# Kernel optimization log

Hardware: AMD Instinct MI355X
Metric: run time of the kernel (lower is better)

The kernel has to match this reference:

```python
import jax, jax.numpy as jnp
import numpy as np
from jax import lax

C = 128
B, H, W = 8, 128, 128
HW = H * W


def _layernorm(x, w, b):
    # x: [b,c,h,w]; WithBias LN over channel dim c (matches to_3d -> LN(last dim=c) -> to_4d)
    mu = jnp.mean(x, axis=1, keepdims=True)
    var = jnp.mean((x - mu) ** 2, axis=1, keepdims=True)
    xn = (x - mu) / jnp.sqrt(var + 1e-5)
    return xn * w[None, :, None, None] + b[None, :, None, None]


def _conv1x1(x, w, b):
    # x: [b,c,h,w], w: [out,in]
    return jnp.einsum('bchw,oc->bohw', x, w) + b[None, :, None, None]


def _dwconv3(x, w, b):
    # depthwise 3x3, w: [c,1,3,3]
    c = x.shape[1]
    y = lax.conv_general_dilated(x, w, window_strides=(1, 1),
                                 padding=((1, 1), (1, 1)),
                                 feature_group_count=c,
                                 dimension_numbers=('NCHW', 'OIHW', 'NCHW'))
    return y + b[None, :, None, None]


def _l2norm(x):
    # torch F.normalize(dim=-1): x / max(||x||, 1e-12)
    n = jnp.sqrt(jnp.sum(x * x, axis=-1, keepdims=True))
    return x / jnp.maximum(n, 1e-12)


def setup_inputs() -> dict:
    key = jax.random.key(0)
    ks = jax.random.split(key, 12)
    s = 0.02
    return {
        'pre': jax.random.normal(ks[0], (B, HW, C), jnp.float32),
        'cur': jax.random.normal(ks[1], (B, HW, C), jnp.float32),
        'ln1_w': jnp.ones((C,), jnp.float32),
        'ln1_b': jnp.zeros((C,), jnp.float32),
        'ln2_w': jnp.ones((C,), jnp.float32),
        'ln2_b': jnp.zeros((C,), jnp.float32),
        'q_w1': jax.random.normal(ks[2], (C, C), jnp.float32) * s,
        'q_b1': jnp.zeros((C,), jnp.float32),
        'q_w2': jax.random.normal(ks[3], (C, 1, 3, 3), jnp.float32) * s,
        'q_b2': jnp.zeros((C,), jnp.float32),
        'kv_w1': jax.random.normal(ks[4], (2 * C, C), jnp.float32) * s,
        'kv_b1': jnp.zeros((2 * C,), jnp.float32),
        'kv_w2': jax.random.normal(ks[5], (2 * C, 1, 3, 3), jnp.float32) * s,
        'kv_b2': jnp.zeros((2 * C,), jnp.float32),
        'out_w': jax.random.normal(ks[6], (C, C), jnp.float32) * s,
        'out_b': jnp.zeros((C,), jnp.float32),
    }


def reference(pre, cur, ln1_w, ln1_b, ln2_w, ln2_b,
              q_w1, q_b1, q_w2, q_b2,
              kv_w1, kv_b1, kv_w2, kv_b2,
              out_w, out_b):
    b, hw, c = cur.shape
    h = w = int(np.sqrt(hw))
    # [b,hw,c] -> [b,c,h,w]
    cur4 = jnp.transpose(cur.reshape(b, h, w, c), (0, 3, 1, 2))
    pre4 = jnp.transpose(pre.reshape(b, h, w, c), (0, 3, 1, 2))

    pre_ln = _layernorm(pre4, ln1_w, ln1_b)
    cur_ln = _layernorm(cur4, ln2_w, ln2_b)

    q = _dwconv3(_conv1x1(cur_ln, q_w1, q_b1), q_w2, q_b2)        # [b,c,h,w]
    kv = _dwconv3(_conv1x1(pre_ln, kv_w1, kv_b1), kv_w2, kv_b2)   # [b,2c,h,w]
    k, v = jnp.split(kv, 2, axis=1)

    q = _l2norm(q.reshape(b, c, hw))
    k = _l2norm(k.reshape(b, c, hw))
    v = v.reshape(b, c, hw)

    att = jax.nn.softmax(jnp.einsum('bcn,bdn->bcd', q, k), axis=-1)  # [b,c,c]
    out = jnp.einsum('bcd,bdn->bcn', att, v).reshape(b, c, h, w)

    out = _conv1x1(out, out_w, out_b) + cur4                         # residual
    # [b,c,h,w] -> [b,hw,c]
    return jnp.transpose(out.reshape(b, c, hw), (0, 2, 1))
```

## Files before the change

kernel.cpp:

```cpp
#include <hip/hip_runtime.h>

typedef __attribute__((ext_vector_type(4))) float f32x4;
typedef __attribute__((ext_vector_type(2))) float f32x2;
typedef __attribute__((ext_vector_type(8))) short s16x8;
typedef __attribute__((ext_vector_type(4))) short s16x4;
typedef __bf16 bf16x8 __attribute__((ext_vector_type(8)));

__device__ __forceinline__ short f2bf(float f) {
  union { float f; unsigned u; } c; c.f = f;
  unsigned r = c.u + 0x7fffu + ((c.u >> 16) & 1u);
  return (short)(r >> 16);
}
__device__ __forceinline__ float bf2f(short s) {
  union { unsigned u; float f; } c; c.u = ((unsigned)(unsigned short)s) << 16;
  return c.f;
}

__global__ void k0_prep(const float* __restrict__ qw1, const float* __restrict__ qb1,
                        const float* __restrict__ kvw1, const float* __restrict__ kvb1,
                        const float* __restrict__ ln1w, const float* __restrict__ ln1b,
                        const float* __restrict__ ln2w, const float* __restrict__ ln2b,
                        short* __restrict__ Wq, short* __restrict__ Wk, short* __restrict__ Wv,
                        float* __restrict__ T)
{
  const int path = blockIdx.x;
  const int o = threadIdx.x >> 1, hf = threadIdx.x & 1;
  const float *W, *bias, *lw, *lb; short* Wo; float *t1, *t2;
  if (path == 0)      { W = qw1;            bias = qb1;       lw = ln2w; lb = ln2b; Wo = Wq; t1 = T;       t2 = T + 128; }
  else if (path == 1) { W = kvw1;           bias = kvb1;      lw = ln1w; lb = ln1b; Wo = Wk; t1 = T + 256; t2 = T + 384; }
  else                { W = kvw1 + 16384;   bias = kvb1+128;  lw = ln1w; lb = ln1b; Wo = Wv; t1 = T + 512; t2 = T + 640; }
  float s1 = 0.f, s2 = 0.f;
  for (int g = 0; g < 64; g++) {
    const int c = hf * 64 + g;
    const float w = W[o * 128 + c];
    const float wp = w * lw[c];
    s1 += wp; s2 += w * lb[c];
    Wo[o * 128 + c] = f2bf(wp);
  }
  s1 += __shfl_xor(s1, 1);
  s2 += __shfl_xor(s2, 1);
  if (hf == 0) { t1[o] = s1; t2[o] = s2 + bias[o]; }
}

__global__ __launch_bounds__(256, 3)
void k1_ln_gemm(const float* __restrict__ cur, const float* __restrict__ pre,
                const short* __restrict__ Wq, const short* __restrict__ Wk,
                const short* __restrict__ Wv, const float* __restrict__ T,
                short* __restrict__ Yq, short* __restrict__ Yk, short* __restrict__ Yv)
{
  __shared__ __attribute__((aligned(16))) short At[128][136];
  __shared__ f32x2 rowstat[128];
  const int tid = threadIdx.x, bx = blockIdx.x;
  const int path = bx >> 10;
  const int mblk = bx & 1023;
  const float* X = (path == 0) ? cur : pre;
  const short* Wp = (path == 0) ? Wq : (path == 1) ? Wk : Wv;
  const float* t1 = T + path * 256;
  const float* t2 = t1 + 128;
  const int b = mblk >> 7;
  const int pl0 = (mblk & 127) * 128;

  {
    const int r = tid >> 1, hf = tid & 1;
    const float* src = X + ((size_t)(mblk * 128 + r)) * 128 + hf * 64;
    float s1 = 0.f, s2 = 0.f;
#pragma unroll
    for (int g = 0; g < 8; g++) {
      const f32x4 v0 = *(const f32x4*)(src + g * 8);
      const f32x4 v1 = *(const f32x4*)(src + g * 8 + 4);
      s16x8 o;
#pragma unroll
      for (int j = 0; j < 4; j++) {
        s1 += v0[j] + v1[j]; s2 += v0[j] * v0[j] + v1[j] * v1[j];
        o[j] = f2bf(v0[j]); o[4 + j] = f2bf(v1[j]);
      }
      *(s16x8*)&At[r][hf * 64 + g * 8] = o;
    }
    s1 += __shfl_xor(s1, 1);
    s2 += __shfl_xor(s2, 1);
    if (hf == 0) {
      const float mu = s1 * (1.f / 128.f);
      const float var = s2 * (1.f / 128.f) - mu * mu;
      rowstat[r] = (f32x2){mu, rsqrtf(var + 1e-5f)};
    }
  }
  __syncthreads();

  const int wv = tid >> 6, lane = tid & 63, l16 = lane & 15, quad = lane >> 4, kof = quad * 8;
  f32x4 acc[2][8];
#pragma unroll
  for (int i = 0; i < 2; i++)
#pragma unroll
    for (int j = 0; j < 8; j++) acc[i][j] = (f32x4){0.f, 0.f, 0.f, 0.f};

  if (path < 2) {
#pragma unroll
    for (int ks = 0; ks < 4; ks++) {
      const int kb = ks * 32 + kof;
      const bf16x8 a0 = *(const bf16x8*)&At[wv * 32 + l16][kb];
      const bf16x8 a1 = *(const bf16x8*)&At[wv * 32 + 16 + l16][kb];
#pragma unroll
      for (int j = 0; j < 8; j++) {
        const bf16x8 bv = *(const bf16x8*)(Wp + (j * 16 + l16) * 128 + kb);
        acc[0][j] = __builtin_amdgcn_mfma_f32_16x16x32_bf16(a0, bv, acc[0][j], 0, 0, 0);
        acc[1][j] = __builtin_amdgcn_mfma_f32_16x16x32_bf16(a1, bv, acc[1][j], 0, 0, 0);
      }
    }
    short* Yout = (path == 0) ? Yq : Yk;
    float t1v[8], t2v[8];
#pragma unroll
    for (int j = 0; j < 8; j++) { const int o = j * 16 + l16; t1v[j] = t1[o]; t2v[j] = t2[o]; }
#pragma unroll
    for (int i = 0; i < 2; i++) {
      const int pr = wv * 32 + i * 16 + quad * 4;
      f32x2 st[4];
#pragma unroll
      for (int rg = 0; rg < 4; rg++) st[rg] = rowstat[pr + rg];
#pragma unroll
      for (int j = 0; j < 8; j++) {
        const int o = j * 16 + l16;
        s16x4 pk;
#pragma unroll
        for (int rg = 0; rg < 4; rg++) {
          const float y = st[rg].y * acc[i][j][rg] - st[rg].x * st[rg].y * t1v[j] + t2v[j];
          pk[rg] = f2bf(y);
        }
        *(s16x4*)(Yout + ((size_t)(b * 128 + o)) * 16384 + pl0 + pr) = pk;
      }
    }
  } else {
#pragma unroll
    for (int ks = 0; ks < 4; ks++) {
      const int kb = ks * 32 + kof;
      const bf16x8 w0 = *(const bf16x8*)(Wp + (wv * 32 + l16) * 128 + kb);
      const bf16x8 w1 = *(const bf16x8*)(Wp + (wv * 32 + 16 + l16) * 128 + kb);
#pragma unroll
      for (int j = 0; j < 8; j++) {
        const bf16x8 xv = *(const bf16x8*)&At[j * 16 + l16][kb];
        acc[0][j] = __builtin_amdgcn_mfma_f32_16x16x32_bf16(w0, xv, acc[0][j], 0, 0, 0);
        acc[1][j] = __builtin_amdgcn_mfma_f32_16x16x32_bf16(w1, xv, acc[1][j], 0, 0, 0);
      }
    }
#pragma unroll
    for (int i = 0; i < 2; i++) {
      const int o0 = wv * 32 + i * 16 + quad * 4;
      const f32x4 t14 = *(const f32x4*)(t1 + o0);
      const f32x4 t24 = *(const f32x4*)(t2 + o0);
#pragma unroll
      for (int j = 0; j < 8; j++) {
        const int pc = j * 16 + l16;
        const f32x2 st = rowstat[pc];
        s16x4 pk;
#pragma unroll
        for (int rg = 0; rg < 4; rg++) {
          const float y = st.y * acc[i][j][rg] - st.x * st.y * t14[rg] + t24[rg];
          pk[rg] = f2bf(y);
        }
        *(s16x4*)(Yv + ((size_t)(mblk * 128 + pc)) * 128 + o0) = pk;
      }
    }
  }
}

__global__ __launch_bounds__(256, 4)
void k2_plane(const short* __restrict__ Yq, const short* __restrict__ Yk,
              const short* __restrict__ Yv,
              const float* __restrict__ qw2, const float* __restrict__ qb2,
              const float* __restrict__ kvw2, const float* __restrict__ kvb2,
              short* __restrict__ qo, short* __restrict__ ko, short* __restrict__ vo,
              float* __restrict__ nq, float* __restrict__ nk)
{
  __shared__ __attribute__((aligned(16))) short tile[130][144];
  __shared__ float red[256];
  const int tid = threadIdx.x, bx = blockIdx.x;
  const int path = bx >> 10, rem = bx & 1023;
  const int b = rem >> 7, c = rem & 127;
  const short* in; const float* w2p; float bsv; short* outp; float* np;
  if (path == 0)      { in = Yq; w2p = qw2 + c * 9;          bsv = qb2[c];        outp = qo; np = nq; }
  else if (path == 1) { in = Yk; w2p = kvw2 + c * 9;         bsv = kvb2[c];       outp = ko; np = nk; }
  else                { in = Yv; w2p = kvw2 + (128 + c) * 9; bsv = kvb2[128 + c]; outp = vo; np = nullptr; }

  const short* plane = in + ((size_t)(b * 128 + c)) * 16384;
#pragma unroll
  for (int g = 0; g < 8; g++) {
    const int e = (g * 256 + tid) * 8;
    *(s16x8*)&tile[(e >> 7) + 1][(e & 127) + 8] = *(const s16x8*)(plane + e);
  }
  const s16x8 z8 = (s16x8){0, 0, 0, 0, 0, 0, 0, 0};
  if (tid < 128) *(s16x8*)&tile[tid + 1][136] = z8;
  if (tid < 36) { const int rr = (tid / 18) * 129, cc = (tid % 18) * 8; *(s16x8*)&tile[rr][cc] = z8; }
  __syncthreads();

  float wt[9];
#pragma unroll
  for (int j = 0; j < 9; j++) wt[j] = w2p[j];
  const int rr = tid >> 1, hfc = tid & 1;

  float A0[8], A1[8], A2[8];
  {
    const int ca = 8 + hfc * 64;
    const s16x8 a0 = *(const s16x8*)&tile[rr][ca];
    const s16x8 a1 = *(const s16x8*)&tile[rr + 1][ca];
    const s16x8 a2 = *(const s16x8*)&tile[rr + 2][ca];
#pragma unroll
    for (int x = 0; x < 8; x++) { A0[x] = bf2f(a0[x]); A1[x] = bf2f(a1[x]); A2[x] = bf2f(a2[x]); }
  }
  float p0, p1, p2;
  if (hfc) { p0 = bf2f(tile[rr][71]); p1 = bf2f(tile[rr + 1][71]); p2 = bf2f(tile[rr + 2][71]); }
  else { p0 = p1 = p2 = 0.f; }

  float ss = 0.f;
  short* oplane = outp + ((size_t)(b * 128 + c)) * 16384 + rr * 128 + hfc * 64;
#pragma unroll
  for (int g = 0; g < 8; g++) {
    const int cb = 16 + hfc * 64 + g * 8;
    const s16x8 b0 = *(const s16x8*)&tile[rr][cb];
    const s16x8 b1 = *(const s16x8*)&tile[rr + 1][cb];
    const s16x8 b2 = *(const s16x8*)&tile[rr + 2][cb];
    float B0[8], B1[8], B2[8];
#pragma unroll
    for (int x = 0; x < 8; x++) { B0[x] = bf2f(b0[x]); B1[x] = bf2f(b1[x]); B2[x] = bf2f(b2[x]); }
    s16x8 ov;
#pragma unroll
    for (int x = 0; x < 8; x++) {
      const float l0 = x ? A0[x - 1] : p0, l1 = x ? A1[x - 1] : p1, l2 = x ? A2[x - 1] : p2;
      const float r0 = (x < 7) ? A0[x + 1] : B0[0];
      const float r1 = (x < 7) ? A1[x + 1] : B1[0];
      const float r2 = (x < 7) ? A2[x + 1] : B2[0];
      float s = bsv;
      s += wt[0] * l0 + wt[1] * A0[x] + wt[2] * r0;
      s += wt[3] * l1 + wt[4] * A1[x] + wt[5] * r1;
      s += wt[6] * l2 + wt[7] * A2[x] + wt[8] * r2;
      ov[x] = f2bf(s); ss += s * s;
    }
    *(s16x8*)(oplane + g * 8) = ov;
    p0 = A0[7]; p1 = A1[7]; p2 = A2[7];
#pragma unroll
    for (int x = 0; x < 8; x++) { A0[x] = B0[x]; A1[x] = B1[x]; A2[x] = B2[x]; }
  }
  red[tid] = ss;
  __syncthreads();
  if (tid < 64) {
    float t = red[tid] + red[tid + 64] + red[tid + 128] + red[tid + 192];
#pragma unroll
    for (int m = 32; m >= 1; m >>= 1) t += __shfl_xor(t, m);
    if (tid == 0 && np) np[b * 128 + c] = t;
  }
}

__global__ __launch_bounds__(256, 2)
void k3_gram(const short* __restrict__ qo, const short* __restrict__ ko,
             float* __restrict__ Gp)
{
  const int tid = threadIdx.x, bx = blockIdx.x;
  const int b = bx >> 6, sp = bx & 63;
  const int wv = tid >> 6, lane = tid & 63, l16 = lane & 15, quad = lane >> 4, kof = quad * 8;
  f32x4 acc[2][8];
#pragma unroll
  for (int i = 0; i < 2; i++)
#pragma unroll
    for (int j = 0; j < 8; j++) acc[i][j] = (f32x4){0.f, 0.f, 0.f, 0.f};

  const short* qb = qo + (size_t)b * 128 * 16384 + sp * 256 + kof;
  const short* kb = ko + (size_t)b * 128 * 16384 + sp * 256 + kof;
#pragma unroll
  for (int ks = 0; ks < 8; ks++) {
    const int n0 = ks * 32;
    const bf16x8 a0 = *(const bf16x8*)(qb + (size_t)(wv * 32 + l16) * 16384 + n0);
    const bf16x8 a1 = *(const bf16x8*)(qb + (size_t)(wv * 32 + 16 + l16) * 16384 + n0);
#pragma unroll
    for (int j = 0; j < 8; j++) {
      const bf16x8 bv = *(const bf16x8*)(kb + (size_t)(j * 16 + l16) * 16384 + n0);
      acc[0][j] = __builtin_amdgcn_mfma_f32_16x16x32_bf16(a0, bv, acc[0][j], 0, 0, 0);
      acc[1][j] = __builtin_amdgcn_mfma_f32_16x16x32_bf16(a1, bv, acc[1][j], 0, 0, 0);
    }
  }
  float* gp = Gp + ((size_t)(sp * 8 + b)) * 16384;
#pragma unroll
  for (int i = 0; i < 2; i++)
#pragma unroll
    for (int j = 0; j < 8; j++)
#pragma unroll
      for (int rg = 0; rg < 4; rg++)
        gp[(wv * 32 + i * 16 + quad * 4 + rg) * 128 + j * 16 + l16] = acc[i][j][rg];
}

__global__ void k4a_softmax(const float* __restrict__ Gp,
                            const float* __restrict__ nq, const float* __restrict__ nk,
                            float* __restrict__ att)
{
  const int tid = threadIdx.x;
  const int b = blockIdx.x >> 4, cb = (blockIdx.x & 15) * 8;
  const int r = tid >> 5, dsi = tid & 31;
  const int c = cb + r, d0 = dsi * 4;
  f32x4 a = (f32x4){0.f, 0.f, 0.f, 0.f};
  for (int ks = 0; ks < 64; ks++)
    a += *(const f32x4*)(Gp + ((size_t)(ks * 8 + b)) * 16384 + c * 128 + d0);
  const float qn = fmaxf(sqrtf(nq[b * 128 + c]), 1e-12f);
  f32x4 sc;
#pragma unroll
  for (int j = 0; j < 4; j++) {
    const float kn = fmaxf(sqrtf(nk[b * 128 + d0 + j]), 1e-12f);
    sc[j] = a[j] / (qn * kn);
  }
  float mx = fmaxf(fmaxf(sc[0], sc[1]), fmaxf(sc[2], sc[3]));
#pragma unroll
  for (int m = 16; m >= 1; m >>= 1) mx = fmaxf(mx, __shfl_xor(mx, m));
  f32x4 e; float sum = 0.f;
#pragma unroll
  for (int j = 0; j < 4; j++) { e[j] = __expf(sc[j] - mx); sum += e[j]; }
#pragma unroll
  for (int m = 16; m >= 1; m >>= 1) sum += __shfl_xor(sum, m);
  const float inv = 1.f / sum;
  f32x4 o;
#pragma unroll
  for (int j = 0; j < 4; j++) o[j] = e[j] * inv;
  *(f32x4*)(att + (size_t)b * 16384 + c * 128 + d0) = o;
}

__global__ void k4b_mw(const float* __restrict__ att, const float* __restrict__ outw,
                       short* __restrict__ Mb)
{
  __shared__ float at[128][8];
  const int tid = threadIdx.x, bx = blockIdx.x;
  const int b = bx >> 4, d0 = (bx & 15) * 8;
  {
    const int cc = tid >> 1, q = tid & 1;
    *(f32x4*)&at[cc][q * 4] = *(const f32x4*)(att + (size_t)b * 16384 + cc * 128 + d0 + q * 4);
  }
  __syncthreads();
  const int o = tid & 127, dq = (tid >> 7) * 4;
  f32x4 acc = (f32x4){0.f, 0.f, 0.f, 0.f};
  const float* wr = outw + o * 128;
  for (int cc = 0; cc < 128; cc++) {
    const float w = wr[cc];
    const f32x4 a = *(const f32x4*)&at[cc][dq];
    acc += w * a;
  }
  s16x4 pk;
#pragma unroll
  for (int rg = 0; rg < 4; rg++) pk[rg] = f2bf(acc[rg]);
  *(s16x4*)(Mb + ((size_t)(b * 128 + o)) * 128 + d0 + dq) = pk;
}

__global__ __launch_bounds__(256, 3)
void k5_out(const short* __restrict__ Mb, const short* __restrict__ vp,
            const float* __restrict__ outb, const float* __restrict__ cur,
            float* __restrict__ out)
{
  __shared__ __attribute__((aligned(16))) short Vt[128][136];
  const int tid = threadIdx.x;
  const int b = blockIdx.x >> 7, nb = (blockIdx.x & 127) * 128;
  {
    const int d = tid >> 1, hf = tid & 1;
    const short* src = vp + ((size_t)(b * 128 + d)) * 16384 + nb + hf * 64;
#pragma unroll
    for (int g = 0; g < 8; g++) {
      const s16x8 v = *(const s16x8*)(src + g * 8);
#pragma unroll
      for (int x = 0; x < 8; x++) Vt[hf * 64 + g * 8 + x][d] = v[x];
    }
  }
  __syncthreads();
  const int wv = tid >> 6, lane = tid & 63, l16 = lane & 15, quad = lane >> 4, kof = quad * 8;
  f32x4 acc[2][8];
#pragma unroll
  for (int i = 0; i < 2; i++)
#pragma unroll
    for (int j = 0; j < 8; j++) acc[i][j] = (f32x4){0.f, 0.f, 0.f, 0.f};

  const short* m0 = Mb + ((size_t)(b * 128 + wv * 32 + l16)) * 128;
  const short* m1 = m0 + 16 * 128;
#pragma unroll
  for (int ks = 0; ks < 4; ks++) {
    const int kb = ks * 32 + kof;
    const bf16x8 a0 = *(const bf16x8*)(m0 + kb);
    const bf16x8 a1 = *(const bf16x8*)(m1 + kb);
#pragma unroll
    for (int j = 0; j < 8; j++) {
      const bf16x8 bv = *(const bf16x8*)&Vt[j * 16 + l16][kb];
      acc[0][j] = __builtin_amdgcn_mfma_f32_16x16x32_bf16(a0, bv, acc[0][j], 0, 0, 0);
      acc[1][j] = __builtin_amdgcn_mfma_f32_16x16x32_bf16(a1, bv, acc[1][j], 0, 0, 0);
    }
  }
#pragma unroll
  for (int i = 0; i < 2; i++) {
    const int o0 = wv * 32 + i * 16 + quad * 4;
    const f32x4 bias = *(const f32x4*)(outb + o0);
#pragma unroll
    for (int j = 0; j < 8; j++) {
      const int pos = nb + j * 16 + l16;
      const size_t idx = ((size_t)(b * 16384 + pos)) * 128 + o0;
      const f32x4 cv = *(const f32x4*)(cur + idx);
      f32x4 rr;
#pragma unroll
      for (int rg = 0; rg < 4; rg++) rr[rg] = acc[i][j][rg] + bias[rg] + cv[rg];
      *(f32x4*)(out + idx) = rr;
    }
  }
}

extern "C" void kernel_launch(void* const* d_in, const int* in_sizes, int n_in,
                              void* d_out, int out_size, void* d_ws, size_t ws_size,
                              hipStream_t stream) {
  const float* pre  = (const float*)d_in[0];
  const float* cur  = (const float*)d_in[1];
  const float* ln1w = (const float*)d_in[2];
  const float* ln1b = (const float*)d_in[3];
  const float* ln2w = (const float*)d_in[4];
  const float* ln2b = (const float*)d_in[5];
  const float* qw1  = (const float*)d_in[6];
  const float* qb1  = (const float*)d_in[7];
  const float* qw2  = (const float*)d_in[8];
  const float* qb2  = (const float*)d_in[9];
  const float* kvw1 = (const float*)d_in[10];
  const float* kvb1 = (const float*)d_in[11];
  const float* kvw2 = (const float*)d_in[12];
  const float* kvb2 = (const float*)d_in[13];
  const float* outw = (const float*)d_in[14];
  const float* outb = (const float*)d_in[15];

  char* ws = (char*)d_ws;
  short* Yq  = (short*)(ws);
  short* Yk  = (short*)(ws + 33554432);
  short* Yv  = (short*)(ws + 67108864);
  short* qo  = (short*)(ws + 100663296);
  short* ko  = (short*)(ws + 134217728);
  short* vo  = (short*)(ws + 167772160);
  float* Gp  = (float*)(ws);
  float* att = (float*)(ws + 33554432);
  short* Mb  = (short*)(ws + 34078720);
  char*  sm  = ws + 201326592;
  short* Wq  = (short*)(sm);
  short* Wk  = (short*)(sm + 32768);
  short* Wv  = (short*)(sm + 65536);
  float* T   = (float*)(sm + 98304);
  float* nq  = (float*)(sm + 102400);
  float* nk  = (float*)(sm + 106496);

  hipLaunchKernelGGL(k0_prep, dim3(3), dim3(256), 0, stream,
                     qw1, qb1, kvw1, kvb1, ln1w, ln1b, ln2w, ln2b, Wq, Wk, Wv, T);
  hipLaunchKernelGGL(k1_ln_gemm, dim3(3072), dim3(256), 0, stream,
                     cur, pre, Wq, Wk, Wv, T, Yq, Yk, Yv);
  hipLaunchKernelGGL(k2_plane, dim3(3072), dim3(256), 0, stream,
                     Yq, Yk, Yv, qw2, qb2, kvw2, kvb2, qo, ko, vo, nq, nk);
  hipLaunchKernelGGL(k3_gram, dim3(512), dim3(256), 0, stream, qo, ko, Gp);
  hipLaunchKernelGGL(k4a_softmax, dim3(128), dim3(256), 0, stream, Gp, nq, nk, att);
  hipLaunchKernelGGL(k4b_mw, dim3(128), dim3(256), 0, stream, att, outw, Mb);
  hipLaunchKernelGGL(k5_out, dim3(1024), dim3(256), 0, stream, Mb, vo, outb, cur, (float*)d_out);
}
```

Before: 406.1 us.

## Share pre-input load across K and V GEMMs and halve gram split-K

The LayerNorm+GEMM kernel now runs 2048 blocks instead of 3072. Each pre-input block loads and converts its tile once, then computes both the K and V projections in two passes, writing V in the same channel-plane layout as K. The tile is loaded with fully coalesced vector reads, and the row statistics are computed from the bf16 copy in shared memory. This slightly changes LayerNorm numerics. The gram kernel now uses 32 split-K chunks instead of 64, which halves partial-sum traffic for the softmax reduction, and two kernels get a higher occupancy hint.

```diff
diff --git a/kernel.cpp b/kernel.cpp
--- a/kernel.cpp
+++ b/kernel.cpp
@@ -42,7 +42,7 @@
   if (hf == 0) { t1[o] = s1; t2[o] = s2 + bias[o]; }
 }
 
-__global__ __launch_bounds__(256, 3)
+__global__ __launch_bounds__(256, 4)
 void k1_ln_gemm(const float* __restrict__ cur, const float* __restrict__ pre,
                 const short* __restrict__ Wq, const short* __restrict__ Wk,
                 const short* __restrict__ Wv, const float* __restrict__ T,
@@ -53,28 +53,31 @@
   const int tid = threadIdx.x, bx = blockIdx.x;
   const int path = bx >> 10;
   const int mblk = bx & 1023;
-  const float* X = (path == 0) ? cur : pre;
-  const short* Wp = (path == 0) ? Wq : (path == 1) ? Wk : Wv;
-  const float* t1 = T + path * 256;
-  const float* t2 = t1 + 128;
+  const float* X = path ? pre : cur;
   const int b = mblk >> 7;
   const int pl0 = (mblk & 127) * 128;
 
   {
+    const float* src = X + (size_t)mblk * 16384;
+    const int r0 = tid >> 5, c0 = (tid & 31) * 4;
+#pragma unroll
+    for (int it = 0; it < 16; it++) {
+      const f32x4 v = *(const f32x4*)(src + it * 1024 + tid * 4);
+      s16x4 o;
+#pragma unroll
+      for (int j = 0; j < 4; j++) o[j] = f2bf(v[j]);
+      *(s16x4*)&At[it * 8 + r0][c0] = o;
+    }
+  }
+  __syncthreads();
+  {
     const int r = tid >> 1, hf = tid & 1;
-    const float* src = X + ((size_t)(mblk * 128 + r)) * 128 + hf * 64;
     float s1 = 0.f, s2 = 0.f;
 #pragma unroll
     for (int g = 0; g < 8; g++) {
-      const f32x4 v0 = *(const f32x4*)(src + g * 8);
-      const f32x4 v1 = *(const f32x4*)(src + g * 8 + 4);
-      s16x8 o;
-#pragma unroll
-      for (int j = 0; j < 4; j++) {
-        s1 += v0[j] + v1[j]; s2 += v0[j] * v0[j] + v1[j] * v1[j];
-        o[j] = f2bf(v0[j]); o[4 + j] = f2bf(v1[j]);
-      }
-      *(s16x8*)&At[r][hf * 64 + g * 8] = o;
+      const s16x8 v = *(const s16x8*)&At[r][hf * 64 + g * 8];
+#pragma unroll
+      for (int x = 0; x < 8; x++) { const float f = bf2f(v[x]); s1 += f; s2 += f * f; }
     }
     s1 += __shfl_xor(s1, 1);
     s2 += __shfl_xor(s2, 1);
@@ -87,13 +90,19 @@
   __syncthreads();
 
   const int wv = tid >> 6, lane = tid & 63, l16 = lane & 15, quad = lane >> 4, kof = quad * 8;
-  f32x4 acc[2][8];
-#pragma unroll
-  for (int i = 0; i < 2; i++)
-#pragma unroll
-    for (int j = 0; j < 8; j++) acc[i][j] = (f32x4){0.f, 0.f, 0.f, 0.f};
-
-  if (path < 2) {
+  const int npass = path ? 2 : 1;
+  for (int ps = 0; ps < npass; ps++) {
+    const short* Wp = path ? (ps ? Wv : Wk) : Wq;
+    short* Yout = path ? (ps ? Yv : Yk) : Yq;
+    const float* t1 = T + (path ? (ps ? 512 : 256) : 0);
+    const float* t2 = t1 + 128;
+
+    f32x4 acc[2][8];
+#pragma unroll
+    for (int i = 0; i < 2; i++)
+#pragma unroll
+      for (int j = 0; j < 8; j++) acc[i][j] = (f32x4){0.f, 0.f, 0.f, 0.f};
+
 #pragma unroll
     for (int ks = 0; ks < 4; ks++) {
       const int kb = ks * 32 + kof;
@@ -106,7 +115,6 @@
         acc[1][j] = __builtin_amdgcn_mfma_f32_16x16x32_bf16(a1, bv, acc[1][j], 0, 0, 0);
       }
     }
-    short* Yout = (path == 0) ? Yq : Yk;
     float t1v[8], t2v[8];
 #pragma unroll
     for (int j = 0; j < 8; j++) { const int o = j * 16 + l16; t1v[j] = t1[o]; t2v[j] = t2[o]; }
@@ -126,37 +134,6 @@
           pk[rg] = f2bf(y);
         }
         *(s16x4*)(Yout + ((size_t)(b * 128 + o)) * 16384 + pl0 + pr) = pk;
-      }
-    }
-  } else {
-#pragma unroll
-    for (int ks = 0; ks < 4; ks++) {
-      const int kb = ks * 32 + kof;
-      const bf16x8 w0 = *(const bf16x8*)(Wp + (wv * 32 + l16) * 128 + kb);
-      const bf16x8 w1 = *(const bf16x8*)(Wp + (wv * 32 + 16 + l16) * 128 + kb);
-#pragma unroll
-      for (int j = 0; j < 8; j++) {
-        const bf16x8 xv = *(const bf16x8*)&At[j * 16 + l16][kb];
-        acc[0][j] = __builtin_amdgcn_mfma_f32_16x16x32_bf16(w0, xv, acc[0][j], 0, 0, 0);
-        acc[1][j] = __builtin_amdgcn_mfma_f32_16x16x32_bf16(w1, xv, acc[1][j], 0, 0, 0);
-      }
-    }
-#pragma unroll
-    for (int i = 0; i < 2; i++) {
-      const int o0 = wv * 32 + i * 16 + quad * 4;
-      const f32x4 t14 = *(const f32x4*)(t1 + o0);
-      const f32x4 t24 = *(const f32x4*)(t2 + o0);
-#pragma unroll
-      for (int j = 0; j < 8; j++) {
-        const int pc = j * 16 + l16;
-        const f32x2 st = rowstat[pc];
-        s16x4 pk;
-#pragma unroll
-        for (int rg = 0; rg < 4; rg++) {
-          const float y = st.y * acc[i][j][rg] - st.x * st.y * t14[rg] + t24[rg];
-          pk[rg] = f2bf(y);
-        }
-        *(s16x4*)(Yv + ((size_t)(mblk * 128 + pc)) * 128 + o0) = pk;
       }
     }
   }
@@ -253,7 +230,7 @@
              float* __restrict__ Gp)
 {
   const int tid = threadIdx.x, bx = blockIdx.x;
-  const int b = bx >> 6, sp = bx & 63;
+  const int b = bx >> 5, sp = bx & 31;
   const int wv = tid >> 6, lane = tid & 63, l16 = lane & 15, quad = lane >> 4, kof = quad * 8;
   f32x4 acc[2][8];
 #pragma unroll
@@ -261,10 +238,10 @@
 #pragma unroll
     for (int j = 0; j < 8; j++) acc[i][j] = (f32x4){0.f, 0.f, 0.f, 0.f};
 
-  const short* qb = qo + (size_t)b * 128 * 16384 + sp * 256 + kof;
-  const short* kb = ko + (size_t)b * 128 * 16384 + sp * 256 + kof;
-#pragma unroll
-  for (int ks = 0; ks < 8; ks++) {
+  const short* qb = qo + (size_t)b * 128 * 16384 + sp * 512 + kof;
+  const short* kb = ko + (size_t)b * 128 * 16384 + sp * 512 + kof;
+#pragma unroll
+  for (int ks = 0; ks < 16; ks++) {
     const int n0 = ks * 32;
     const bf16x8 a0 = *(const bf16x8*)(qb + (size_t)(wv * 32 + l16) * 16384 + n0);
     const bf16x8 a1 = *(const bf16x8*)(qb + (size_t)(wv * 32 + 16 + l16) * 16384 + n0);
@@ -294,7 +271,7 @@
   const int r = tid >> 5, dsi = tid & 31;
   const int c = cb + r, d0 = dsi * 4;
   f32x4 a = (f32x4){0.f, 0.f, 0.f, 0.f};
-  for (int ks = 0; ks < 64; ks++)
+  for (int ks = 0; ks < 32; ks++)
     a += *(const f32x4*)(Gp + ((size_t)(ks * 8 + b)) * 16384 + c * 128 + d0);
   const float qn = fmaxf(sqrtf(nq[b * 128 + c]), 1e-12f);
   f32x4 sc;
@@ -343,7 +320,7 @@
   *(s16x4*)(Mb + ((size_t)(b * 128 + o)) * 128 + d0 + dq) = pk;
 }
 
-__global__ __launch_bounds__(256, 3)
+__global__ __launch_bounds__(256, 4)
 void k5_out(const short* __restrict__ Mb, const short* __restrict__ vp,
             const float* __restrict__ outb, const float* __restrict__ cur,
             float* __restrict__ out)
@@ -440,11 +417,11 @@
 
   hipLaunchKernelGGL(k0_prep, dim3(3), dim3(256), 0, stream,
                      qw1, qb1, kvw1, kvb1, ln1w, ln1b, ln2w, ln2b, Wq, Wk, Wv, T);
-  hipLaunchKernelGGL(k1_ln_gemm, dim3(3072), dim3(256), 0, stream,
+  hipLaunchKernelGGL(k1_ln_gemm, dim3(2048), dim3(256), 0, stream,
                      cur, pre, Wq, Wk, Wv, T, Yq, Yk, Yv);
   hipLaunchKernelGGL(k2_plane, dim3(3072), dim3(256), 0, stream,
                      Yq, Yk, Yv, qw2, qb2, kvw2, kvb2, qo, ko, vo, nq, nk);
-  hipLaunchKernelGGL(k3_gram, dim3(512), dim3(256), 0, stream, qo, ko, Gp);
+  hipLaunchKernelGGL(k3_gram, dim3(256), dim3(256), 0, stream, qo, ko, Gp);
   hipLaunchKernelGGL(k4a_softmax, dim3(128), dim3(256), 0, stream, Gp, nq, nk, att);
   hipLaunchKernelGGL(k4b_mw, dim3(128), dim3(256), 0, stream, att, outw, Mb);
   hipLaunchKernelGGL(k5_out, dim3(1024), dim3(256), 0, stream, Mb, vo, outb, cur, (float*)d_out);
```

New measurement: 463.7 us. +14.2%, slower.
